# Performance work log

Hardware: AMD Instinct MI355X
Metric: run time of the kernel (lower is better)

The kernel has to match this reference:

```python
import jax, jax.numpy as jnp
import numpy as np

B, SEQ, VOCAB = 128, 200, 1400
D = 256          # input_size == hidden_size
H = 256
NCLS = 128


def _p(key, shape, scale=0.05):
    return jax.random.normal(key, shape, dtype=jnp.float32) * scale


def setup_inputs() -> dict:
    key = jax.random.key(0)
    ks = jax.random.split(key, 24)
    inp = {
        "inputs": jax.random.uniform(ks[0], (B, SEQ, VOCAB), dtype=jnp.float32),
        "timestamps": jax.random.uniform(ks[1], (B, SEQ), dtype=jnp.float32),
        "emb": _p(ks[2], (VOCAB, D)),
        # TimeLSTM 1
        "Wall1_w": _p(ks[3], (4 * H, D)), "Wall1_b": _p(ks[4], (4 * H,)),
        "Uall1_w": _p(ks[5], (4 * H, H)), "Uall1_b": _p(ks[6], (4 * H,)),
        "Wd1_w": _p(ks[7], (H, H)), "Wd1_b": _p(ks[8], (H,)),
        # TimeLSTM 2
        "Wall2_w": _p(ks[9], (4 * H, D)), "Wall2_b": _p(ks[10], (4 * H,)),
        "Uall2_w": _p(ks[11], (4 * H, H)), "Uall2_b": _p(ks[12], (4 * H,)),
        "Wd2_w": _p(ks[13], (H, H)), "Wd2_b": _p(ks[14], (H,)),
        # attention / output heads
        "wa_w": _p(ks[15], (1, H)),
        "Wb_w": _p(ks[16], (H, H)),
        "Wout_w": _p(ks[17], (NCLS, H)),
        # initial states (torch.randn in original forward)
        "h01": jax.random.normal(ks[18], (B, H), dtype=jnp.float32),
        "c01": jax.random.normal(ks[19], (B, H), dtype=jnp.float32),
        "h02": jax.random.normal(ks[20], (B, H), dtype=jnp.float32),
        "c02": jax.random.normal(ks[21], (B, H), dtype=jnp.float32),
    }
    return inp


def _time_lstm(embedded, timestamps, h0, c0, Wall_w, Wall_b, Uall_w, Uall_b, Wd_w, Wd_b):
    # Precompute the input projection for all steps (one big GEMM).
    # NOTE: original code applies W_all to h and U_all to x.
    ux = jnp.einsum('bsd,ed->sbe', embedded, Uall_w) + Uall_b  # [seq, b, 4h]
    ts = jnp.swapaxes(timestamps, 0, 1)[:, :, None]            # [seq, b, 1]

    def step(carry, xs):
        h, c = carry
        ux_s, t_s = xs
        c_s1 = jnp.tanh(c @ Wd_w.T + Wd_b)
        c_adj = c - c_s1 + c_s1 * t_s
        gates = jax.nn.sigmoid(h @ Wall_w.T + Wall_b + ux_s)   # all 4 gates sigmoid (incl. c_tmp)
        f, i, o, c_tmp = jnp.split(gates, 4, axis=1)
        c_new = f * c_adj + i * c_tmp
        h_new = o * jnp.tanh(c_new)
        return (h_new, c_new), h_new

    _, hs = jax.lax.scan(step, (h0, c0), (ux, ts))
    return jnp.swapaxes(hs, 0, 1)  # [b, seq, h]


def reference(inputs, timestamps, emb,
              Wall1_w, Wall1_b, Uall1_w, Uall1_b, Wd1_w, Wd1_b,
              Wall2_w, Wall2_b, Uall2_w, Uall2_b, Wd2_w, Wd2_b,
              wa_w, Wb_w, Wout_w, h01, c01, h02, c02):
    embedded = jnp.einsum('bsv,vd->bsd', inputs, emb)  # [b, seq, d]
    out1 = _time_lstm(embedded, timestamps, h01, c01,
                      Wall1_w, Wall1_b, Uall1_w, Uall1_b, Wd1_w, Wd1_b)
    E = jnp.einsum('bsh,h->bs', out1, wa_w[0])
    alpha = jax.nn.softmax(E, axis=1)                  # [b, seq]
    out2 = _time_lstm(embedded, timestamps, h02, c02,
                      Wall2_w, Wall2_b, Uall2_w, Uall2_b, Wd2_w, Wd2_b)
    Beta = jnp.tanh(jnp.einsum('bsh,kh->bsk', out2, Wb_w))  # [b, seq, h]
    ctx = jnp.sum(embedded * Beta * alpha[:, :, None], axis=1)  # [b, h]
    return ctx @ Wout_w.T  # [b, num_classes]
```

## Files before the change

kernel.cpp:

```cpp
#include <hip/hip_runtime.h>

typedef unsigned short u16;
typedef unsigned int u32;
typedef unsigned long long u64;
typedef __attribute__((ext_vector_type(8))) short bf16x8;
typedef __attribute__((ext_vector_type(4))) float f32x4;
typedef __attribute__((ext_vector_type(4))) unsigned short us4;

#define MFMA(a,b,c) __builtin_amdgcn_mfma_f32_16x16x32_bf16((a),(b),(c),0,0,0)
#define KEEP(x) asm volatile("" : "+v"(x))


static __device__ __forceinline__ u16 f2b(float f){
  unsigned u = __float_as_uint(f);
  u += 0x7fffu + ((u >> 16) & 1u);
  return (u16)(u >> 16);
}
static __device__ __forceinline__ float sigm(float x){ return 1.0f/(1.0f+__expf(-x)); }
static __device__ __forceinline__ float tanhx(float x){
  x = fminf(fmaxf(x, -15.f), 15.f);
  float e = __expf(-2.f*x);
  return (1.f - e)/(1.f + e);
}
static __device__ __forceinline__ void gl16(const void* g, void* l){
  __builtin_amdgcn_global_load_lds((const __attribute__((address_space(1))) void*)g,
                                   (__attribute__((address_space(3))) void*)l, 16, 0, 0);
}

__global__ __launch_bounds__(256) void k_prep(
  const float* __restrict__ in0, u16* __restrict__ A0,
  const float* __restrict__ emb, u16* __restrict__ embT,
  const float* __restrict__ s0, const float* __restrict__ s1, const float* __restrict__ s2,
  const float* __restrict__ s3, const float* __restrict__ s4, const float* __restrict__ s5,
  const float* __restrict__ s6,
  u16* __restrict__ d0, u16* __restrict__ d1, u16* __restrict__ d2, u16* __restrict__ d3,
  u16* __restrict__ d4, u16* __restrict__ d5, u16* __restrict__ d6)
{
  int bx = blockIdx.x, tid = threadIdx.x;
  if (bx < 35200){
    long long i4 = (long long)bx*256 + tid;
    long long o = i4*4;
    int r = (int)(o / 1408);
    int c = (int)(o % 1408);
    us4 d;
    if (c + 4 <= 1400){
      f32x4 v = *(const f32x4*)&in0[(long long)r*1400 + c];
      d[0]=f2b(v[0]); d[1]=f2b(v[1]); d[2]=f2b(v[2]); d[3]=f2b(v[3]);
    } else {
      for (int k=0;k<4;k++){ int cc=c+k; d[k] = (cc<1400)? f2b(in0[(long long)r*1400+cc]) : (u16)0; }
    }
    *(us4*)&A0[(long long)r*1408 + c] = d;
  } else if (bx < 36608){
    int idx = (bx-35200)*256 + tid;
    int n = idx / 1408, k = idx % 1408;
    embT[idx] = (k < 1400) ? f2b(emb[(long long)k*256 + n]) : (u16)0;
  } else {
    long long q = (long long)(bx-36608)*256 + tid;
    const float* src; u16* dst; long long rel;
    if      (q < 65536)  { src=s0; dst=d0; rel=q; }
    else if (q < 131072) { src=s1; dst=d1; rel=q-65536; }
    else if (q < 196608) { src=s2; dst=d2; rel=q-131072; }
    else if (q < 262144) { src=s3; dst=d3; rel=q-196608; }
    else if (q < 278528) { src=s4; dst=d4; rel=q-262144; }
    else if (q < 294912) { src=s5; dst=d5; rel=q-278528; }
    else                 { src=s6; dst=d6; rel=q-294912; }
    long long o = rel*4;
    f32x4 v = *(const f32x4*)&src[o];
    us4 d; d[0]=f2b(v[0]); d[1]=f2b(v[1]); d[2]=f2b(v[2]); d[3]=f2b(v[3]);
    *(us4*)&dst[o] = d;
  }
}

__global__ __launch_bounds__(256) void k_init(float* __restrict__ E, float* __restrict__ ctx,
                                              int* __restrict__ fl){
  int i = blockIdx.x*256 + threadIdx.x;
  if (i < 25600) E[i] = 0.f;
  else if (i < 58368) ctx[i-25600] = 0.f;
  else fl[i-58368] = 0;
}

template<int EPI>
__global__ __launch_bounds__(256) void k_gemm(const u16* __restrict__ A, const u16* __restrict__ Bt,
    int N, int K,
    float* __restrict__ Cf, u16* __restrict__ Cb,
    const float* __restrict__ bias1, const float* __restrict__ bias2,
    const u16* __restrict__ Bt2, float* __restrict__ Cf2,
    const float* __restrict__ bias3, const float* __restrict__ bias4,
    const float* __restrict__ emb, const float* __restrict__ alpha)
{
  __shared__ __align__(16) u16 As[128*64];
  __shared__ __align__(16) u16 Bs[128*64];
  __shared__ float red[2][128];
  const int tid = threadIdx.x;
  const int l = tid & 63, w = tid >> 6;
  const int quad = l >> 4, lb = l & 15;
  const int wr = w >> 1, wc = w & 1;
  const long long m0 = (long long)blockIdx.x * 128;
  int n0 = blockIdx.y * 128;
  if (EPI==4 && blockIdx.y >= 8){
    Bt = Bt2; Cf = Cf2; bias1 = bias3; bias2 = bias4; n0 = (blockIdx.y-8)*128;
  }

  f32x4 acc[4][4];
  #pragma unroll
  for (int i=0;i<4;i++)
    #pragma unroll
    for (int j=0;j<4;j++) acc[i][j] = (f32x4){0.f,0.f,0.f,0.f};

  for (int kk = 0; kk < K; kk += 64){
    #pragma unroll
    for (int it=0; it<4; ++it){
      int slot = it*256 + tid;
      int m = slot >> 3;
      int q = (slot & 7) ^ (m & 7);
      gl16(A + (m0+m)*K + kk + q*8, &As[slot*8]);
    }
    #pragma unroll
    for (int it=0; it<4; ++it){
      int slot = it*256 + tid;
      int m = slot >> 3;
      int q = (slot & 7) ^ (m & 7);
      gl16(Bt + (long long)(n0+m)*K + kk + q*8, &Bs[slot*8]);
    }
    __syncthreads();
    #pragma unroll
    for (int ks=0; ks<2; ++ks){
      int kq = quad + ks*4;
      bf16x8 af[4], bfr[4];
      #pragma unroll
      for (int i=0;i<4;i++){ int m = wr*64 + i*16 + lb; af[i]  = *(const bf16x8*)&As[m*64 + ((kq ^ (m&7))*8)]; }
      #pragma unroll
      for (int j=0;j<4;j++){ int n = wc*64 + j*16 + lb; bfr[j] = *(const bf16x8*)&Bs[n*64 + ((kq ^ (n&7))*8)]; }
      #pragma unroll
      for (int i=0;i<4;i++)
        #pragma unroll
        for (int j=0;j<4;j++)
          acc[i][j] = MFMA(af[i], bfr[j], acc[i][j]);
    }
    __syncthreads();
  }

  if (EPI==5){
    const int b0 = (int)(m0 / 200);
    red[tid>>7][tid&127] = 0.f;
    __syncthreads();
    #pragma unroll
    for (int i=0;i<4;i++){
      #pragma unroll
      for (int j=0;j<4;j++){
        int col = wc*64 + j*16 + lb;
        #pragma unroll
        for (int r=0;r<4;r++){
          long long row = m0 + wr*64 + i*16 + quad*4 + r;
          long long o = row*N + n0 + col;
          float v = emb[o] * tanhx(acc[i][j][r]) * alpha[row];
          atomicAdd(&red[(int)(row/200) - b0][col], v);
        }
      }
    }
    __syncthreads();
    int bl = tid >> 7, col = tid & 127;
    int bb = b0 + bl;
    if (bb < 128) atomicAdd(&Cf[bb*256 + n0 + col], red[bl][col]);
    return;
  }

  #pragma unroll
  for (int i=0;i<4;i++){
    #pragma unroll
    for (int j=0;j<4;j++){
      int col = n0 + wc*64 + j*16 + lb;
      #pragma unroll
      for (int r=0;r<4;r++){
        long long row = m0 + wr*64 + i*16 + quad*4 + r;
        long long o = row*N + col;
        float v = acc[i][j][r];
        if (EPI==1){ Cf[o]=v; Cb[o]=f2b(v); }
        else { Cf[o] = v + bias1[col] + bias2[col]; }
      }
    }
  }
}

__global__ __launch_bounds__(256,1) void k_scan(
  const u16* __restrict__ Wall1, const u16* __restrict__ Wd1, const float* __restrict__ Wd1b,
  const float* __restrict__ ux1, const float* __restrict__ h01, const float* __restrict__ c01,
  const u16* __restrict__ Wall2, const u16* __restrict__ Wd2, const float* __restrict__ Wd2b,
  const float* __restrict__ ux2, const float* __restrict__ h02, const float* __restrict__ c02,
  const float* __restrict__ ts, const float* __restrict__ wa,
  float* __restrict__ E, u16* __restrict__ out2,
  u64* __restrict__ mb, int* __restrict__ fl)
{
  __shared__ __align__(16) u16 hb[16][264];
  __shared__ __align__(16) u16 cb[16][264];
  const int bi = blockIdx.x;
  const int jw   = bi >> 4;
  const int grp  = bi & 15;
  const int lstm = (bi >> 3) & 1;
  const int bc   = bi & 7;
  const u16* Wall  = lstm ? Wall2 : Wall1;
  const u16* Wd    = lstm ? Wd2   : Wd1;
  const float* Wdb = lstm ? Wd2b  : Wd1b;
  const float* ux  = lstm ? ux2   : ux1;
  const float* h0  = lstm ? h02   : h01;
  const float* c0  = lstm ? c02   : c01;

  const int tid = threadIdx.x;
  const int l = tid & 63, w = tid >> 6;
  const int quad = l >> 4, lb = l & 15;
  const int bg = bc*16 + lb;
  const int jwave = jw*64 + w*16;
  const int jlane = jwave + quad*4;

  bf16x8 wfA[4][8], wdA[8];
  #pragma unroll
  for (int g=0; g<4; ++g)
    #pragma unroll
    for (int kk=0; kk<8; ++kk){
      wfA[g][kk] = *(const bf16x8*)&Wall[(long long)(g*256 + jwave + lb)*256 + kk*32 + quad*8];
      KEEP(wfA[g][kk]);
    }
  #pragma unroll
  for (int kk=0; kk<8; ++kk){
    wdA[kk] = *(const bf16x8*)&Wd[(long long)(jwave + lb)*256 + kk*32 + quad*8];
    KEEP(wdA[kk]);
  }

  f32x4 bcs  = *(const f32x4*)&Wdb[jlane];
  f32x4 wav  = *(const f32x4*)&wa[jlane];
  f32x4 creg = *(const f32x4*)&c0[(long long)bg*256 + jlane];

  {
    const int bbi = tid >> 4, j0i = (tid & 15) * 16;
    #pragma unroll
    for (int kq=0; kq<4; ++kq){
      f32x4 hv = *(const f32x4*)&h0[(long long)(bc*16+bbi)*256 + j0i + kq*4];
      f32x4 cv = *(const f32x4*)&c0[(long long)(bc*16+bbi)*256 + j0i + kq*4];
      us4 hp0, cp0;
      #pragma unroll
      for (int r=0;r<4;++r){ hp0[r]=f2b(hv[r]); cp0[r]=f2b(cv[r]); }
      *(us4*)&hb[bbi][j0i+kq*4] = hp0;
      *(us4*)&cb[bbi][j0i+kq*4] = cp0;
    }
  }
  __syncthreads();

  f32x4 uxr[4];
  #pragma unroll
  for (int g=0; g<4; ++g)
    uxr[g] = *(const f32x4*)&ux[(long long)bg*200*1024 + g*256 + jlane];
  float tcur = ts[(long long)bg*200];

  for (int s=0; s<200; ++s){
    f32x4 ag[4];
    #pragma unroll
    for (int g=0; g<4; ++g) ag[g] = uxr[g];
    float tnext = tcur;
    if (s < 199){
      #pragma unroll
      for (int g=0; g<4; ++g)
        uxr[g] = *(const f32x4*)&ux[((long long)bg*200 + s+1)*1024 + g*256 + jlane];
      tnext = ts[(long long)bg*200 + s+1];
    }
    f32x4 ad = bcs;
    #pragma unroll
    for (int kk=0;kk<8;++kk){
      bf16x8 cf = *(const bf16x8*)&cb[lb][kk*32 + quad*8];
      ad = MFMA(wdA[kk], cf, ad);
    }
    #pragma unroll
    for (int kk=0;kk<8;++kk){
      bf16x8 hf = *(const bf16x8*)&hb[lb][kk*32 + quad*8];
      #pragma unroll
      for (int g=0; g<4; ++g) ag[g] = MFMA(wfA[g][kk], hf, ag[g]);
    }
    f32x4 hn; us4 hp, cp;
    #pragma unroll
    for (int r=0;r<4;++r){
      float cs1 = tanhx(ad[r]);
      float cadj = creg[r] + cs1*(tcur - 1.0f);
      float fg = sigm(ag[0][r]);
      float ig = sigm(ag[1][r]);
      float og = sigm(ag[2][r]);
      float cg = sigm(ag[3][r]);
      float cn = fg*cadj + ig*cg;
      float hv = og*tanhx(cn);
      creg[r]=cn; hn[r]=hv;
      hp[r]=f2b(hv); cp[r]=f2b(cn);
    }

    if (s < 199){
      const int slot = (s+1)&1;
      {
        long long xb = ((long long)((((slot*16+grp)*4 + jw)*4 + w)))*128 + l*2;
        u64 w0 = (u64)((u32)hp[0] | ((u32)cp[0]<<16)) | ((u64)((u32)hp[1] | ((u32)cp[1]<<16))<<32);
        u64 w1 = (u64)((u32)hp[2] | ((u32)cp[2]<<16)) | ((u64)((u32)hp[3] | ((u32)cp[3]<<16))<<32);
        __hip_atomic_store(&mb[xb],   w0, __ATOMIC_RELAXED, __HIP_MEMORY_SCOPE_AGENT);
        __hip_atomic_store(&mb[xb+1], w1, __ATOMIC_RELAXED, __HIP_MEMORY_SCOPE_AGENT);
      }
      asm volatile("s_waitcnt vmcnt(0)" ::: "memory");
      if (l == 0)
        __hip_atomic_store(&fl[(grp*4 + jw)*4 + w], s+1, __ATOMIC_RELAXED, __HIP_MEMORY_SCOPE_AGENT);
      asm volatile("" ::: "memory");
      __builtin_amdgcn_s_barrier();
      asm volatile("" ::: "memory");
      *(us4*)&hb[lb][jlane] = hp;
      *(us4*)&cb[lb][jlane] = cp;
      {
        const u32 tgt = (u32)(s+1);
        const int sj = (jw + 1 + l) & 3;
        const int* fp = &fl[(grp*4 + sj)*4 + w];
        for (;;){
          u32 fv = tgt;
          if (l < 3) fv = (u32)__hip_atomic_load(fp, __ATOMIC_RELAXED, __HIP_MEMORY_SCOPE_AGENT);
          if (__all((int)(fv >= tgt))) break;
        }
      }
      u64 d0a, d0b, d1a, d1b, d2a, d2b;
      {
        const int j1 = (jw+1)&3, j2 = (jw+2)&3, j3 = (jw+3)&3;
        long long rb1 = ((long long)((((slot*16+grp)*4 + j1)*4 + w)))*128 + l*2;
        long long rb2 = ((long long)((((slot*16+grp)*4 + j2)*4 + w)))*128 + l*2;
        long long rb3 = ((long long)((((slot*16+grp)*4 + j3)*4 + w)))*128 + l*2;
        d0a = __hip_atomic_load(&mb[rb1],   __ATOMIC_RELAXED, __HIP_MEMORY_SCOPE_AGENT);
        d0b = __hip_atomic_load(&mb[rb1+1], __ATOMIC_RELAXED, __HIP_MEMORY_SCOPE_AGENT);
        d1a = __hip_atomic_load(&mb[rb2],   __ATOMIC_RELAXED, __HIP_MEMORY_SCOPE_AGENT);
        d1b = __hip_atomic_load(&mb[rb2+1], __ATOMIC_RELAXED, __HIP_MEMORY_SCOPE_AGENT);
        d2a = __hip_atomic_load(&mb[rb3],   __ATOMIC_RELAXED, __HIP_MEMORY_SCOPE_AGENT);
        d2b = __hip_atomic_load(&mb[rb3+1], __ATOMIC_RELAXED, __HIP_MEMORY_SCOPE_AGENT);
      }
      if (lstm==0){
        float e = hn[0]*wav[0] + hn[1]*wav[1] + hn[2]*wav[2] + hn[3]*wav[3];
        e += __shfl_xor(e, 16, 64);
        e += __shfl_xor(e, 32, 64);
        if (l < 16) atomicAdd(&E[(long long)bg*200 + s], e);
      } else {
        *(us4*)&out2[((long long)bg*200 + s)*256 + jlane] = hp;
      }
      {
        const int j1 = (jw+1)&3, j2 = (jw+2)&3, j3 = (jw+3)&3;
        us4 hh, cc;
        u32 lo, hi;
        lo=(u32)d0a; hi=(u32)(d0a>>32); hh[0]=(u16)lo; cc[0]=(u16)(lo>>16); hh[1]=(u16)hi; cc[1]=(u16)(hi>>16);
        lo=(u32)d0b; hi=(u32)(d0b>>32); hh[2]=(u16)lo; cc[2]=(u16)(lo>>16); hh[3]=(u16)hi; cc[3]=(u16)(hi>>16);
        *(us4*)&hb[lb][j1*64 + w*16 + quad*4] = hh;
        *(us4*)&cb[lb][j1*64 + w*16 + quad*4] = cc;
        lo=(u32)d1a; hi=(u32)(d1a>>32); hh[0]=(u16)lo; cc[0]=(u16)(lo>>16); hh[1]=(u16)hi; cc[1]=(u16)(hi>>16);
        lo=(u32)d1b; hi=(u32)(d1b>>32); hh[2]=(u16)lo; cc[2]=(u16)(lo>>16); hh[3]=(u16)hi; cc[3]=(u16)(hi>>16);
        *(us4*)&hb[lb][j2*64 + w*16 + quad*4] = hh;
        *(us4*)&cb[lb][j2*64 + w*16 + quad*4] = cc;
        lo=(u32)d2a; hi=(u32)(d2a>>32); hh[0]=(u16)lo; cc[0]=(u16)(lo>>16); hh[1]=(u16)hi; cc[1]=(u16)(hi>>16);
        lo=(u32)d2b; hi=(u32)(d2b>>32); hh[2]=(u16)lo; cc[2]=(u16)(lo>>16); hh[3]=(u16)hi; cc[3]=(u16)(hi>>16);
        *(us4*)&hb[lb][j3*64 + w*16 + quad*4] = hh;
        *(us4*)&cb[lb][j3*64 + w*16 + quad*4] = cc;
      }
      asm volatile("s_waitcnt lgkmcnt(0)" ::: "memory");
      __builtin_amdgcn_sched_barrier(0);
      __builtin_amdgcn_s_barrier();
      asm volatile("" ::: "memory");
      tcur = tnext;
    } else {
      if (lstm==0){
        float e = hn[0]*wav[0] + hn[1]*wav[1] + hn[2]*wav[2] + hn[3]*wav[3];
        e += __shfl_xor(e, 16, 64);
        e += __shfl_xor(e, 32, 64);
        if (l < 16) atomicAdd(&E[(long long)bg*200 + s], e);
      } else {
        *(us4*)&out2[((long long)bg*200 + s)*256 + jlane] = hp;
      }
    }
  }
}

__global__ __launch_bounds__(256) void k_attn(const float* __restrict__ E, float* __restrict__ alpha){
  __shared__ float buf[256];
  int b = blockIdx.x, tid = threadIdx.x;
  float Ev = (tid < 200) ? E[(long long)b*200 + tid] : -1e30f;
  buf[tid]=Ev; __syncthreads();
  for (int st=128; st>0; st>>=1){ if (tid<st) buf[tid]=fmaxf(buf[tid],buf[tid+st]); __syncthreads(); }
  float mx = buf[0]; __syncthreads();
  float e = (tid<200)? __expf(Ev-mx) : 0.f;
  buf[tid]=e; __syncthreads();
  for (int st=128; st>0; st>>=1){ if (tid<st) buf[tid]+=buf[tid+st]; __syncthreads(); }
  float sm = buf[0];
  if (tid<200) alpha[(long long)b*200+tid] = e/sm;
}

__global__ __launch_bounds__(128) void k_out(const float* __restrict__ ctx, const float* __restrict__ Wout,
                                             float* __restrict__ out){
  __shared__ float cs[256];
  int b = blockIdx.x, t = threadIdx.x;
  cs[t] = ctx[b*256+t]; cs[t+128] = ctx[b*256+t+128];
  __syncthreads();
  const float* wr = Wout + (long long)t*256;
  float a0=0,a1=0,a2=0,a3=0;
  for (int j=0;j<256;j+=4){
    f32x4 v = *(const f32x4*)&wr[j];
    a0+=v[0]*cs[j]; a1+=v[1]*cs[j+1]; a2+=v[2]*cs[j+2]; a3+=v[3]*cs[j+3];
  }
  out[(long long)b*128 + t] = (a0+a1)+(a2+a3);
}

extern "C" void kernel_launch(void* const* d_in, const int* in_sizes, int n_in,
                              void* d_out, int out_size, void* d_ws, size_t ws_size,
                              hipStream_t stream)
{
  (void)in_sizes; (void)n_in; (void)out_size; (void)ws_size;
  const float* inputs = (const float*)d_in[0];
  const float* tstamp = (const float*)d_in[1];
  const float* emb    = (const float*)d_in[2];
  const float* Wall1w = (const float*)d_in[3];
  const float* Wall1b = (const float*)d_in[4];
  const float* Uall1w = (const float*)d_in[5];
  const float* Uall1b = (const float*)d_in[6];
  const float* Wd1w   = (const float*)d_in[7];
  const float* Wd1b   = (const float*)d_in[8];
  const float* Wall2w = (const float*)d_in[9];
  const float* Wall2b = (const float*)d_in[10];
  const float* Uall2w = (const float*)d_in[11];
  const float* Uall2b = (const float*)d_in[12];
  const float* Wd2w   = (const float*)d_in[13];
  const float* Wd2b   = (const float*)d_in[14];
  const float* wa     = (const float*)d_in[15];
  const float* Wbw    = (const float*)d_in[16];
  const float* Woutw  = (const float*)d_in[17];
  const float* h01    = (const float*)d_in[18];
  const float* c01    = (const float*)d_in[19];
  const float* h02    = (const float*)d_in[20];
  const float* c02    = (const float*)d_in[21];

  char* ws = (char*)d_ws;
  float* ux1   = (float*)(ws + 0);
  float* ux2   = (float*)(ws + 104857600LL);
  float* embF  = (float*)(ws + 209715200LL);
  u16*   embB  = (u16*)  (ws + 235929600LL);
  char*  scr   =          ws + 249036800LL;
  u16*   A0    = (u16*)scr;
  u16*   out2  = (u16*)  (scr + 0);
  float* alpha = (float*)(scr + 39321600LL);
  float* ctx   = (float*)(scr + 39424000LL);
  float* E     = (float*)(scr + 39555072LL);
  u64*   mb    = (u64*)  (scr + 39657472LL);
  int*   fl    = (int*)  (scr + 40181760LL);
  u16* embT    = (u16*)(ws + 321126400LL);
  u16* Wall1B  = (u16*)(ws + 321847296LL);
  u16* Wall2B  = (u16*)(ws + 322371584LL);
  u16* Uall1B  = (u16*)(ws + 322895872LL);
  u16* Uall2B  = (u16*)(ws + 323420160LL);
  u16* Wd1B    = (u16*)(ws + 323944448LL);
  u16* Wd2B    = (u16*)(ws + 324075520LL);
  u16* WbB     = (u16*)(ws + 324206592LL);

  k_prep<<<37824, 256, 0, stream>>>(inputs, A0, emb, embT,
                                    Wall1w, Wall2w, Uall1w, Uall2w, Wd1w, Wd2w, Wbw,
                                    Wall1B, Wall2B, Uall1B, Uall2B, Wd1B, Wd2B, WbB);
  k_gemm<1><<<dim3(200,2), 256, 0, stream>>>(A0, embT, 256, 1408, embF, embB,
                                             nullptr, nullptr, nullptr, nullptr,
                                             nullptr, nullptr, nullptr, nullptr);
  k_gemm<4><<<dim3(200,16), 256, 0, stream>>>(embB, Uall1B, 1024, 256, ux1, nullptr,
                                              Uall1b, Wall1b,
                                              Uall2B, ux2, Uall2b, Wall2b,
                                              nullptr, nullptr);
  k_init<<<229, 256, 0, stream>>>(E, ctx, fl);
  k_scan<<<64, 256, 0, stream>>>(Wall1B, Wd1B, Wd1b, ux1, h01, c01,
                                 Wall2B, Wd2B, Wd2b, ux2, h02, c02,
                                 tstamp, wa, E, out2, mb, fl);
  k_attn<<<128, 256, 0, stream>>>(E, alpha);
  k_gemm<5><<<dim3(200,2), 256, 0, stream>>>(out2, WbB, 256, 256, ctx, nullptr,
                                             nullptr, nullptr, nullptr, nullptr,
                                             nullptr, nullptr, embF, alpha);
  k_out<<<128, 128, 0, stream>>>(ctx, Woutw, (float*)d_out);
}
```

Before: 1.073 ms.

## Interleave both TimeLSTM recurrences in one workgroup to overlap exchange latency

Each scan workgroup now runs both LSTMs for the same batch chunk and hidden slice, so the launch drops from 64 workgroups to 32. While one LSTM's hidden/cell state is being published and awaited across workgroups, the other LSTM's MFMA work runs, which is meant to hide cross-workgroup synchronization latency behind compute. In exchange each wave holds twice the weight registers (two full sets of Wall and Wd fragments), which risks register spilling, and half as many CUs are used, so per-step compute on each CU roughly doubles.

```diff
diff --git a/kernel.cpp b/kernel.cpp
--- a/kernel.cpp
+++ b/kernel.cpp
@@ -191,19 +191,14 @@
   float* __restrict__ E, u16* __restrict__ out2,
   u64* __restrict__ mb, int* __restrict__ fl)
 {
-  __shared__ __align__(16) u16 hb[16][264];
-  __shared__ __align__(16) u16 cb[16][264];
+  __shared__ __align__(16) u16 hb0[16][264];
+  __shared__ __align__(16) u16 cb0[16][264];
+  __shared__ __align__(16) u16 hb1[16][264];
+  __shared__ __align__(16) u16 cb1[16][264];
   const int bi = blockIdx.x;
-  const int jw   = bi >> 4;
-  const int grp  = bi & 15;
-  const int lstm = (bi >> 3) & 1;
-  const int bc   = bi & 7;
-  const u16* Wall  = lstm ? Wall2 : Wall1;
-  const u16* Wd    = lstm ? Wd2   : Wd1;
-  const float* Wdb = lstm ? Wd2b  : Wd1b;
-  const float* ux  = lstm ? ux2   : ux1;
-  const float* h0  = lstm ? h02   : h01;
-  const float* c0  = lstm ? c02   : c01;
+  const int jw = bi >> 3;
+  const int bc = bi & 7;
+  const int grpA = bc, grpB = 8 + bc;
 
   const int tid = threadIdx.x;
   const int l = tid & 63, w = tid >> 6;
@@ -212,104 +207,174 @@
   const int jwave = jw*64 + w*16;
   const int jlane = jwave + quad*4;
 
-  bf16x8 wfA[4][8], wdA[8];
+  bf16x8 wf0[4][8], wdf0[8], wf1[4][8], wdf1[8];
   #pragma unroll
   for (int g=0; g<4; ++g)
     #pragma unroll
     for (int kk=0; kk<8; ++kk){
-      wfA[g][kk] = *(const bf16x8*)&Wall[(long long)(g*256 + jwave + lb)*256 + kk*32 + quad*8];
-      KEEP(wfA[g][kk]);
+      wf0[g][kk] = *(const bf16x8*)&Wall1[(long long)(g*256 + jwave + lb)*256 + kk*32 + quad*8];
+      KEEP(wf0[g][kk]);
+      wf1[g][kk] = *(const bf16x8*)&Wall2[(long long)(g*256 + jwave + lb)*256 + kk*32 + quad*8];
+      KEEP(wf1[g][kk]);
     }
   #pragma unroll
   for (int kk=0; kk<8; ++kk){
-    wdA[kk] = *(const bf16x8*)&Wd[(long long)(jwave + lb)*256 + kk*32 + quad*8];
-    KEEP(wdA[kk]);
-  }
-
-  f32x4 bcs  = *(const f32x4*)&Wdb[jlane];
+    wdf0[kk] = *(const bf16x8*)&Wd1[(long long)(jwave + lb)*256 + kk*32 + quad*8];
+    KEEP(wdf0[kk]);
+    wdf1[kk] = *(const bf16x8*)&Wd2[(long long)(jwave + lb)*256 + kk*32 + quad*8];
+    KEEP(wdf1[kk]);
+  }
+
+  f32x4 bcs0 = *(const f32x4*)&Wd1b[jlane];
+  f32x4 bcs1 = *(const f32x4*)&Wd2b[jlane];
   f32x4 wav  = *(const f32x4*)&wa[jlane];
-  f32x4 creg = *(const f32x4*)&c0[(long long)bg*256 + jlane];
+  f32x4 creg0 = *(const f32x4*)&c01[(long long)bg*256 + jlane];
+  f32x4 creg1 = *(const f32x4*)&c02[(long long)bg*256 + jlane];
 
   {
     const int bbi = tid >> 4, j0i = (tid & 15) * 16;
     #pragma unroll
     for (int kq=0; kq<4; ++kq){
-      f32x4 hv = *(const f32x4*)&h0[(long long)(bc*16+bbi)*256 + j0i + kq*4];
-      f32x4 cv = *(const f32x4*)&c0[(long long)(bc*16+bbi)*256 + j0i + kq*4];
-      us4 hp0, cp0;
-      #pragma unroll
-      for (int r=0;r<4;++r){ hp0[r]=f2b(hv[r]); cp0[r]=f2b(cv[r]); }
-      *(us4*)&hb[bbi][j0i+kq*4] = hp0;
-      *(us4*)&cb[bbi][j0i+kq*4] = cp0;
+      f32x4 hv0 = *(const f32x4*)&h01[(long long)(bc*16+bbi)*256 + j0i + kq*4];
+      f32x4 cv0 = *(const f32x4*)&c01[(long long)(bc*16+bbi)*256 + j0i + kq*4];
+      f32x4 hv1 = *(const f32x4*)&h02[(long long)(bc*16+bbi)*256 + j0i + kq*4];
+      f32x4 cv1 = *(const f32x4*)&c02[(long long)(bc*16+bbi)*256 + j0i + kq*4];
+      us4 a, b, c, d;
+      #pragma unroll
+      for (int r=0;r<4;++r){ a[r]=f2b(hv0[r]); b[r]=f2b(cv0[r]); c[r]=f2b(hv1[r]); d[r]=f2b(cv1[r]); }
+      *(us4*)&hb0[bbi][j0i+kq*4] = a;
+      *(us4*)&cb0[bbi][j0i+kq*4] = b;
+      *(us4*)&hb1[bbi][j0i+kq*4] = c;
+      *(us4*)&cb1[bbi][j0i+kq*4] = d;
     }
   }
   __syncthreads();
 
-  f32x4 uxr[4];
+  f32x4 uxr0[4], uxr1[4];
   #pragma unroll
-  for (int g=0; g<4; ++g)
-    uxr[g] = *(const f32x4*)&ux[(long long)bg*200*1024 + g*256 + jlane];
+  for (int g=0; g<4; ++g){
+    uxr0[g] = *(const f32x4*)&ux1[(long long)bg*200*1024 + g*256 + jlane];
+    uxr1[g] = *(const f32x4*)&ux2[(long long)bg*200*1024 + g*256 + jlane];
+  }
   float tcur = ts[(long long)bg*200];
 
   for (int s=0; s<200; ++s){
-    f32x4 ag[4];
-    #pragma unroll
-    for (int g=0; g<4; ++g) ag[g] = uxr[g];
-    float tnext = tcur;
+    const int slot = (s+1)&1;
+    const float tnow = tcur;
+
+    f32x4 ag0[4];
+    #pragma unroll
+    for (int g=0; g<4; ++g) ag0[g] = uxr0[g];
     if (s < 199){
       #pragma unroll
       for (int g=0; g<4; ++g)
-        uxr[g] = *(const f32x4*)&ux[((long long)bg*200 + s+1)*1024 + g*256 + jlane];
-      tnext = ts[(long long)bg*200 + s+1];
-    }
-    f32x4 ad = bcs;
+        uxr0[g] = *(const f32x4*)&ux1[((long long)bg*200 + s+1)*1024 + g*256 + jlane];
+    }
+    f32x4 ad0 = bcs0;
     #pragma unroll
     for (int kk=0;kk<8;++kk){
-      bf16x8 cf = *(const bf16x8*)&cb[lb][kk*32 + quad*8];
-      ad = MFMA(wdA[kk], cf, ad);
+      bf16x8 cf = *(const bf16x8*)&cb0[lb][kk*32 + quad*8];
+      ad0 = MFMA(wdf0[kk], cf, ad0);
     }
     #pragma unroll
     for (int kk=0;kk<8;++kk){
-      bf16x8 hf = *(const bf16x8*)&hb[lb][kk*32 + quad*8];
-      #pragma unroll
-      for (int g=0; g<4; ++g) ag[g] = MFMA(wfA[g][kk], hf, ag[g]);
-    }
-    f32x4 hn; us4 hp, cp;
+      bf16x8 hf = *(const bf16x8*)&hb0[lb][kk*32 + quad*8];
+      #pragma unroll
+      for (int g=0; g<4; ++g) ag0[g] = MFMA(wf0[g][kk], hf, ag0[g]);
+    }
+    f32x4 hn0; us4 hp0, cp0;
     #pragma unroll
     for (int r=0;r<4;++r){
-      float cs1 = tanhx(ad[r]);
-      float cadj = creg[r] + cs1*(tcur - 1.0f);
-      float fg = sigm(ag[0][r]);
-      float ig = sigm(ag[1][r]);
-      float og = sigm(ag[2][r]);
-      float cg = sigm(ag[3][r]);
+      float cs1 = tanhx(ad0[r]);
+      float cadj = creg0[r] + cs1*(tnow - 1.0f);
+      float fg = sigm(ag0[0][r]);
+      float ig = sigm(ag0[1][r]);
+      float og = sigm(ag0[2][r]);
+      float cg = sigm(ag0[3][r]);
       float cn = fg*cadj + ig*cg;
       float hv = og*tanhx(cn);
-      creg[r]=cn; hn[r]=hv;
-      hp[r]=f2b(hv); cp[r]=f2b(cn);
-    }
-
+      creg0[r]=cn; hn0[r]=hv;
+      hp0[r]=f2b(hv); cp0[r]=f2b(cn);
+    }
     if (s < 199){
-      const int slot = (s+1)&1;
-      {
-        long long xb = ((long long)((((slot*16+grp)*4 + jw)*4 + w)))*128 + l*2;
-        u64 w0 = (u64)((u32)hp[0] | ((u32)cp[0]<<16)) | ((u64)((u32)hp[1] | ((u32)cp[1]<<16))<<32);
-        u64 w1 = (u64)((u32)hp[2] | ((u32)cp[2]<<16)) | ((u64)((u32)hp[3] | ((u32)cp[3]<<16))<<32);
-        __hip_atomic_store(&mb[xb],   w0, __ATOMIC_RELAXED, __HIP_MEMORY_SCOPE_AGENT);
-        __hip_atomic_store(&mb[xb+1], w1, __ATOMIC_RELAXED, __HIP_MEMORY_SCOPE_AGENT);
-      }
+      long long xb = ((long long)((((slot*16+grpA)*4 + jw)*4 + w)))*128 + l*2;
+      u64 w0 = (u64)((u32)hp0[0] | ((u32)cp0[0]<<16)) | ((u64)((u32)hp0[1] | ((u32)cp0[1]<<16))<<32);
+      u64 w1 = (u64)((u32)hp0[2] | ((u32)cp0[2]<<16)) | ((u64)((u32)hp0[3] | ((u32)cp0[3]<<16))<<32);
+      __hip_atomic_store(&mb[xb],   w0, __ATOMIC_RELAXED, __HIP_MEMORY_SCOPE_AGENT);
+      __hip_atomic_store(&mb[xb+1], w1, __ATOMIC_RELAXED, __HIP_MEMORY_SCOPE_AGENT);
+    }
+
+    f32x4 ag1[4];
+    #pragma unroll
+    for (int g=0; g<4; ++g) ag1[g] = uxr1[g];
+    if (s < 199){
+      #pragma unroll
+      for (int g=0; g<4; ++g)
+        uxr1[g] = *(const f32x4*)&ux2[((long long)bg*200 + s+1)*1024 + g*256 + jlane];
+      tcur = ts[(long long)bg*200 + s+1];
+    }
+    f32x4 ad1 = bcs1;
+    #pragma unroll
+    for (int kk=0;kk<8;++kk){
+      bf16x8 cf = *(const bf16x8*)&cb1[lb][kk*32 + quad*8];
+      ad1 = MFMA(wdf1[kk], cf, ad1);
+    }
+    #pragma unroll
+    for (int kk=0;kk<8;++kk){
+      bf16x8 hf = *(const bf16x8*)&hb1[lb][kk*32 + quad*8];
+      #pragma unroll
+      for (int g=0; g<4; ++g) ag1[g] = MFMA(wf1[g][kk], hf, ag1[g]);
+    }
+    if (s < 199){
       asm volatile("s_waitcnt vmcnt(0)" ::: "memory");
       if (l == 0)
-        __hip_atomic_store(&fl[(grp*4 + jw)*4 + w], s+1, __ATOMIC_RELAXED, __HIP_MEMORY_SCOPE_AGENT);
+        __hip_atomic_store(&fl[(grpA*4 + jw)*4 + w], s+1, __ATOMIC_RELAXED, __HIP_MEMORY_SCOPE_AGENT);
+    }
+    f32x4 hn1; us4 hp1, cp1;
+    #pragma unroll
+    for (int r=0;r<4;++r){
+      float cs1 = tanhx(ad1[r]);
+      float cadj = creg1[r] + cs1*(tnow - 1.0f);
+      float fg = sigm(ag1[0][r]);
+      float ig = sigm(ag1[1][r]);
+      float og = sigm(ag1[2][r]);
+      float cg = sigm(ag1[3][r]);
+      float cn = fg*cadj + ig*cg;
+      float hv = og*tanhx(cn);
+      creg1[r]=cn; hn1[r]=hv;
+      hp1[r]=f2b(hv); cp1[r]=f2b(cn);
+    }
+    if (s < 199){
+      long long xb = ((long long)((((slot*16+grpB)*4 + jw)*4 + w)))*128 + l*2;
+      u64 w0 = (u64)((u32)hp1[0] | ((u32)cp1[0]<<16)) | ((u64)((u32)hp1[1] | ((u32)cp1[1]<<16))<<32);
+      u64 w1 = (u64)((u32)hp1[2] | ((u32)cp1[2]<<16)) | ((u64)((u32)hp1[3] | ((u32)cp1[3]<<16))<<32);
+      __hip_atomic_store(&mb[xb],   w0, __ATOMIC_RELAXED, __HIP_MEMORY_SCOPE_AGENT);
+      __hip_atomic_store(&mb[xb+1], w1, __ATOMIC_RELAXED, __HIP_MEMORY_SCOPE_AGENT);
+      asm volatile("s_waitcnt vmcnt(0)" ::: "memory");
+      if (l == 0)
+        __hip_atomic_store(&fl[(grpB*4 + jw)*4 + w], s+1, __ATOMIC_RELAXED, __HIP_MEMORY_SCOPE_AGENT);
+    }
+
+    {
+      float e = hn0[0]*wav[0] + hn0[1]*wav[1] + hn0[2]*wav[2] + hn0[3]*wav[3];
+      e += __shfl_xor(e, 16, 64);
+      e += __shfl_xor(e, 32, 64);
+      if (l < 16) atomicAdd(&E[(long long)bg*200 + s], e);
+      *(us4*)&out2[((long long)bg*200 + s)*256 + jlane] = hp1;
+    }
+
+    if (s < 199){
       asm volatile("" ::: "memory");
       __builtin_amdgcn_s_barrier();
       asm volatile("" ::: "memory");
-      *(us4*)&hb[lb][jlane] = hp;
-      *(us4*)&cb[lb][jlane] = cp;
+      *(us4*)&hb0[lb][jlane] = hp0;
+      *(us4*)&cb0[lb][jlane] = cp0;
+      *(us4*)&hb1[lb][jlane] = hp1;
+      *(us4*)&cb1[lb][jlane] = cp1;
+      const u32 tgt = (u32)(s+1);
+      const int sj = (jw + 1 + l) & 3;
       {
-        const u32 tgt = (u32)(s+1);
-        const int sj = (jw + 1 + l) & 3;
-        const int* fp = &fl[(grp*4 + sj)*4 + w];
+        const int* fp = &fl[(grpA*4 + sj)*4 + w];
         for (;;){
           u32 fv = tgt;
           if (l < 3) fv = (u32)__hip_atomic_load(fp, __ATOMIC_RELAXED, __HIP_MEMORY_SCOPE_AGENT);
@@ -319,9 +384,9 @@
       u64 d0a, d0b, d1a, d1b, d2a, d2b;
       {
         const int j1 = (jw+1)&3, j2 = (jw+2)&3, j3 = (jw+3)&3;
-        long long rb1 = ((long long)((((slot*16+grp)*4 + j1)*4 + w)))*128 + l*2;
-        long long rb2 = ((long long)((((slot*16+grp)*4 + j2)*4 + w)))*128 + l*2;
-        long long rb3 = ((long long)((((slot*16+grp)*4 + j3)*4 + w)))*128 + l*2;
+        long long rb1 = ((long long)((((slot*16+grpA)*4 + j1)*4 + w)))*128 + l*2;
+        long long rb2 = ((long long)((((slot*16+grpA)*4 + j2)*4 + w)))*128 + l*2;
+        long long rb3 = ((long long)((((slot*16+grpA)*4 + j3)*4 + w)))*128 + l*2;
         d0a = __hip_atomic_load(&mb[rb1],   __ATOMIC_RELAXED, __HIP_MEMORY_SCOPE_AGENT);
         d0b = __hip_atomic_load(&mb[rb1+1], __ATOMIC_RELAXED, __HIP_MEMORY_SCOPE_AGENT);
         d1a = __hip_atomic_load(&mb[rb2],   __ATOMIC_RELAXED, __HIP_MEMORY_SCOPE_AGENT);
@@ -329,45 +394,65 @@
         d2a = __hip_atomic_load(&mb[rb3],   __ATOMIC_RELAXED, __HIP_MEMORY_SCOPE_AGENT);
         d2b = __hip_atomic_load(&mb[rb3+1], __ATOMIC_RELAXED, __HIP_MEMORY_SCOPE_AGENT);
       }
-      if (lstm==0){
-        float e = hn[0]*wav[0] + hn[1]*wav[1] + hn[2]*wav[2] + hn[3]*wav[3];
-        e += __shfl_xor(e, 16, 64);
-        e += __shfl_xor(e, 32, 64);
-        if (l < 16) atomicAdd(&E[(long long)bg*200 + s], e);
-      } else {
-        *(us4*)&out2[((long long)bg*200 + s)*256 + jlane] = hp;
-      }
+      {
+        const int* fp = &fl[(grpB*4 + sj)*4 + w];
+        for (;;){
+          u32 fv = tgt;
+          if (l < 3) fv = (u32)__hip_atomic_load(fp, __ATOMIC_RELAXED, __HIP_MEMORY_SCOPE_AGENT);
+          if (__all((int)(fv >= tgt))) break;
+        }
+      }
+      u64 e0a, e0b, e1a, e1b, e2a, e2b;
       {
         const int j1 = (jw+1)&3, j2 = (jw+2)&3, j3 = (jw+3)&3;
-        us4 hh, cc;
-        u32 lo, hi;
+        long long rb1 = ((long long)((((slot*16+grpB)*4 + j1)*4 + w)))*128 + l*2;
+        long long rb2 = ((long long)((((slot*16+grpB)*4 + j2)*4 + w)))*128 + l*2;
+        long long rb3 = ((long long)((((slot*16+grpB)*4 + j3)*4 + w)))*128 + l*2;
+        e0a = __hip_atomic_load(&mb[rb1],   __ATOMIC_RELAXED, __HIP_MEMORY_SCOPE_AGENT);
+        e0b = __hip_atomic_load(&mb[rb1+1], __ATOMIC_RELAXED, __HIP_MEMORY_SCOPE_AGENT);
+        e1a = __hip_atomic_load(&mb[rb2],   __ATOMIC_RELAXED, __HIP_MEMORY_SCOPE_AGENT);
+        e1b = __hip_atomic_load(&mb[rb2+1], __ATOMIC_RELAXED, __HIP_MEMORY_SCOPE_AGENT);
+        e2a = __hip_atomic_load(&mb[rb3],   __ATOMIC_RELAXED, __HIP_MEMORY_SCOPE_AGENT);
+        e2b = __hip_atomic_load(&mb[rb3+1], __ATOMIC_RELAXED, __HIP_MEMORY_SCOPE_AGENT);
+      }
+      {
+        const int j1 = (jw+1)&3, j2 = (jw+2)&3, j3 = (jw+3)&3;
+        const int rc = w*16 + quad*4;
+        us4 hh, cc; u32 lo, hi;
         lo=(u32)d0a; hi=(u32)(d0a>>32); hh[0]=(u16)lo; cc[0]=(u16)(lo>>16); hh[1]=(u16)hi; cc[1]=(u16)(hi>>16);
         lo=(u32)d0b; hi=(u32)(d0b>>32); hh[2]=(u16)lo; cc[2]=(u16)(lo>>16); hh[3]=(u16)hi; cc[3]=(u16)(hi>>16);
-        *(us4*)&hb[lb][j1*64 + w*16 + quad*4] = hh;
-        *(us4*)&cb[lb][j1*64 + w*16 + quad*4] = cc;
+        *(us4*)&hb0[lb][j1*64 + rc] = hh;
+        *(us4*)&cb0[lb][j1*64 + rc] = cc;
         lo=(u32)d1a; hi=(u32)(d1a>>32); hh[0]=(u16)lo; cc[0]=(u16)(lo>>16); hh[1]=(u16)hi; cc[1]=(u16)(hi>>16);
         lo=(u32)d1b; hi=(u32)(d1b>>32); hh[2]=(u16)lo; cc[2]=(u16)(lo>>16); hh[3]=(u16)hi; cc[3]=(u16)(hi>>16);
-        *(us4*)&hb[lb][j2*64 + w*16 + quad*4] = hh;
-        *(us4*)&cb[lb][j2*64 + w*16 + quad*4] = cc;
+        *(us4*)&hb0[lb][j2*64 + rc] = hh;
+        *(us4*)&cb0[lb][j2*64 + rc] = cc;
         lo=(u32)d2a; hi=(u32)(d2a>>32); hh[0]=(u16)lo; cc[0]=(u16)(lo>>16); hh[1]=(u16)hi; cc[1]=(u16)(hi>>16);
         lo=(u32)d2b; hi=(u32)(d2b>>32); hh[2]=(u16)lo; cc[2]=(u16)(lo>>16); hh[3]=(u16)hi; cc[3]=(u16)(hi>>16);
-        *(us4*)&hb[lb][j3*64 + w*16 + quad*4] = hh;
-        *(us4*)&cb[lb][j3*64 + w*16 + quad*4] = cc;
+        *(us4*)&hb0[lb][j3*64 + rc] = hh;
+        *(us4*)&cb0[lb][j3*64 + rc] = cc;
+      }
+      {
+        const int j1 = (jw+1)&3, j2 = (jw+2)&3, j3 = (jw+3)&3;
+        const int rc = w*16 + quad*4;
+        us4 hh, cc; u32 lo, hi;
+        lo=(u32)e0a; hi=(u32)(e0a>>32); hh[0]=(u16)lo; cc[0]=(u16)(lo>>16); hh[1]=(u16)hi; cc[1]=(u16)(hi>>16);
+        lo=(u32)e0b; hi=(u32)(e0b>>32); hh[2]=(u16)lo; cc[2]=(u16)(lo>>16); hh[3]=(u16)hi; cc[3]=(u16)(hi>>16);
+        *(us4*)&hb1[lb][j1*64 + rc] = hh;
+        *(us4*)&cb1[lb][j1*64 + rc] = cc;
+        lo=(u32)e1a; hi=(u32)(e1a>>32); hh[0]=(u16)lo; cc[0]=(u16)(lo>>16); hh[1]=(u16)hi; cc[1]=(u16)(hi>>16);
+        lo=(u32)e1b; hi=(u32)(e1b>>32); hh[2]=(u16)lo; cc[2]=(u16)(lo>>16); hh[3]=(u16)hi; cc[3]=(u16)(hi>>16);
+        *(us4*)&hb1[lb][j2*64 + rc] = hh;
+        *(us4*)&cb1[lb][j2*64 + rc] = cc;
+        lo=(u32)e2a; hi=(u32)(e2a>>32); hh[0]=(u16)lo; cc[0]=(u16)(lo>>16); hh[1]=(u16)hi; cc[1]=(u16)(hi>>16);
+        lo=(u32)e2b; hi=(u32)(e2b>>32); hh[2]=(u16)lo; cc[2]=(u16)(lo>>16); hh[3]=(u16)hi; cc[3]=(u16)(hi>>16);
+        *(us4*)&hb1[lb][j3*64 + rc] = hh;
+        *(us4*)&cb1[lb][j3*64 + rc] = cc;
       }
       asm volatile("s_waitcnt lgkmcnt(0)" ::: "memory");
       __builtin_amdgcn_sched_barrier(0);
       __builtin_amdgcn_s_barrier();
       asm volatile("" ::: "memory");
-      tcur = tnext;
-    } else {
-      if (lstm==0){
-        float e = hn[0]*wav[0] + hn[1]*wav[1] + hn[2]*wav[2] + hn[3]*wav[3];
-        e += __shfl_xor(e, 16, 64);
-        e += __shfl_xor(e, 32, 64);
-        if (l < 16) atomicAdd(&E[(long long)bg*200 + s], e);
-      } else {
-        *(us4*)&out2[((long long)bg*200 + s)*256 + jlane] = hp;
-      }
     }
   }
 }
@@ -462,7 +547,7 @@
                                               Uall2B, ux2, Uall2b, Wall2b,
                                               nullptr, nullptr);
   k_init<<<229, 256, 0, stream>>>(E, ctx, fl);
-  k_scan<<<64, 256, 0, stream>>>(Wall1B, Wd1B, Wd1b, ux1, h01, c01,
+  k_scan<<<32, 256, 0, stream>>>(Wall1B, Wd1B, Wd1b, ux1, h01, c01,
                                  Wall2B, Wd2B, Wd2b, ux2, h02, c02,
                                  tstamp, wa, E, out2, mb, fl);
   k_attn<<<128, 256, 0, stream>>>(E, alpha);
```

New measurement: 1.536 ms. +43.1%, slower.
